# Kernel optimization log

Measured on AMD Instinct MI355X. Metric: run time of the kernel, lower is better.

Reference implementation:

```python
import jax, jax.numpy as jnp
import numpy as np

N_NODES = 50000
N_EDGES = 1600000
D = 128
L = 4
N_GRAPHS = 512


def setup_inputs() -> dict:
    key = jax.random.key(0)
    ks = jax.random.split(key, 8)
    x = jax.random.normal(ks[0], (N_NODES, D), dtype=jnp.float32)
    edge_index = jax.random.randint(ks[1], (2, N_EDGES), 0, N_NODES, dtype=jnp.int64)
    batch = jnp.sort(jax.random.randint(ks[2], (N_NODES,), 0, N_GRAPHS, dtype=jnp.int64))
    # MLP params per GIN layer: Linear(D->D), ReLU, Linear(D->D). Stacked over L layers.
    s = 1.0 / np.sqrt(D)
    Ws1 = jax.random.uniform(ks[3], (L, D, D), jnp.float32, -s, s)
    bs1 = jax.random.uniform(ks[4], (L, D), jnp.float32, -s, s)
    Ws2 = jax.random.uniform(ks[5], (L, D, D), jnp.float32, -s, s)
    bs2 = jax.random.uniform(ks[6], (L, D), jnp.float32, -s, s)
    return {"x": x, "edge_index": edge_index, "batch": batch,
            "Ws1": Ws1, "bs1": bs1, "Ws2": Ws2, "bs2": bs2}


def reference(x, edge_index, batch, Ws1, bs1, Ws2, bs2):
    src, dst = edge_index[0], edge_index[1]
    for l in range(L):
        # GINConv (eps=0): h = MLP(x + sum_{j in N(i)} x_j)
        agg = jax.ops.segment_sum(x[src], dst, num_segments=N_NODES)  # [N, D]
        h = x + agg
        h = jax.nn.relu(h @ Ws1[l] + bs1[l])
        x = h @ Ws2[l] + bs2[l]
    # global_add_pool: segment-sum node features by graph id
    return jax.ops.segment_sum(x, batch, num_segments=N_GRAPHS)  # [G, D]
```

## Files before the change

kernel.cpp:

```cpp
#include <hip/hip_runtime.h>

#define NN 50000
#define NE 1600000
#define DD 128
#define NL 4
#define NG 512
#define NBUK 196
#define NBLK 196
#define EPB 8192
#define HN (NBUK * NBLK)
#define HT 151

typedef __attribute__((ext_vector_type(8))) short short8;
typedef __attribute__((ext_vector_type(4))) float floatx4;

__device__ __forceinline__ unsigned short f2bf(float f) {
    unsigned int u = __float_as_uint(f);
    u += 0x7fffu + ((u >> 16) & 1u);
    return (unsigned short)(u >> 16);
}
__device__ __forceinline__ float bf2f(unsigned short u) {
    return __uint_as_float(((unsigned int)u) << 16);
}

__global__ __launch_bounds__(256) void cvt_kernel(const float* __restrict__ x,
                                                  unsigned short* __restrict__ xbf) {
    int idx = blockIdx.x * 256 + threadIdx.x;
    float4 f = ((const float4*)x)[idx];
    ushort4 o;
    o.x = f2bf(f.x); o.y = f2bf(f.y); o.z = f2bf(f.z); o.w = f2bf(f.w);
    ((ushort4*)xbf)[idx] = o;
}


__global__ __launch_bounds__(512) void bhist_kernel(const int* __restrict__ dst,
                                                    int* __restrict__ hist) {
    __shared__ int h[NBUK];
    int tid = threadIdx.x;
    for (int i = tid; i < NBUK; i += 512) h[i] = 0;
    __syncthreads();
    int base = blockIdx.x * EPB;
#pragma unroll
    for (int it = 0; it < EPB / 512; it++) {
        int e = base + it * 512 + tid;
        if (e < NE) atomicAdd(&h[dst[e] >> 8], 1);
    }
    __syncthreads();
    for (int i = tid; i < NBUK; i += 512) hist[i * NBLK + blockIdx.x] = h[i];
}

__global__ __launch_bounds__(256) void sum_tiles_kernel(const int* __restrict__ in,
                                                        int* __restrict__ tsum, int n) {
    int i = blockIdx.x * 256 + threadIdx.x;
    __shared__ int s[256];
    s[threadIdx.x] = (i < n) ? in[i] : 0;
    __syncthreads();
    for (int off = 128; off > 0; off >>= 1) {
        if (threadIdx.x < off) s[threadIdx.x] += s[threadIdx.x + off];
        __syncthreads();
    }
    if (threadIdx.x == 0) tsum[blockIdx.x] = s[0];
}

__global__ __launch_bounds__(256) void scan_tiles_kernel(const int* __restrict__ tsum,
                                                         int* __restrict__ toff, int ntiles) {
    int t = threadIdx.x;
    __shared__ int s[256];
    int v = (t < ntiles) ? tsum[t] : 0;
    s[t] = v;
    __syncthreads();
    for (int off = 1; off < 256; off <<= 1) {
        int u = (t >= off) ? s[t - off] : 0;
        __syncthreads();
        s[t] += u;
        __syncthreads();
    }
    if (t < ntiles) toff[t] = s[t] - v;
}

__global__ __launch_bounds__(256) void scan_out_kernel(const int* __restrict__ in,
                                                       const int* __restrict__ toff,
                                                       int* __restrict__ out, int n) {
    int i = blockIdx.x * 256 + threadIdx.x;
    int t = threadIdx.x;
    int v = (i < n) ? in[i] : 0;
    __shared__ int s[256];
    s[t] = v;
    __syncthreads();
    for (int off = 1; off < 256; off <<= 1) {
        int u = (t >= off) ? s[t - off] : 0;
        __syncthreads();
        s[t] += u;
        __syncthreads();
    }
    if (i < n) out[i] = toff[blockIdx.x] + s[t] - v;
}

__global__ __launch_bounds__(512) void bscatter_kernel(const int* __restrict__ src,
                                                       const int* __restrict__ dst,
                                                       const int* __restrict__ bkoff,
                                                       int* __restrict__ ebuf) {
    __shared__ int h[NBUK];
    int tid = threadIdx.x;
    for (int i = tid; i < NBUK; i += 512) h[i] = 0;
    __syncthreads();
    int base = blockIdx.x * EPB;
#pragma unroll
    for (int it = 0; it < EPB / 512; it++) {
        int e = base + it * 512 + tid;
        if (e < NE) {
            int d = dst[e];
            int bu = d >> 8;
            int p = atomicAdd(&h[bu], 1);
            ebuf[bkoff[bu * NBLK + blockIdx.x] + p] = (src[e] << 8) | (d & 255);
        }
    }
}

__global__ __launch_bounds__(256) void bucket_csr_kernel(const int* __restrict__ ebuf,
                                                         const int* __restrict__ bkoff,
                                                         int* __restrict__ rowptr,
                                                         int* __restrict__ col) {
    __shared__ int cnt[256], exc[256], c2[256];
    int b = blockIdx.x, tid = threadIdx.x;
    int segstart = bkoff[b * NBLK];
    int segend = (b < NBUK - 1) ? bkoff[(b + 1) * NBLK] : NE;
    cnt[tid] = 0;
    c2[tid] = 0;
    __syncthreads();
    for (int i = segstart + tid; i < segend; i += 256)
        atomicAdd(&cnt[ebuf[i] & 255], 1);
    __syncthreads();
    int v = cnt[tid];
    exc[tid] = v;
    __syncthreads();
    for (int off = 1; off < 256; off <<= 1) {
        int u = (tid >= off) ? exc[tid - off] : 0;
        __syncthreads();
        exc[tid] += u;
        __syncthreads();
    }
    int excl = exc[tid] - v;
    exc[tid] = excl;
    int node = (b << 8) + tid;
    if (node <= NN) rowptr[node] = segstart + excl;
    __syncthreads();
    for (int i = segstart + tid; i < segend; i += 256) {
        int ev = ebuf[i];
        int low = ev & 255;
        int p = atomicAdd(&c2[low], 1);
        col[segstart + exc[low] + p] = ((unsigned)ev) >> 8;
    }
}

__global__ __launch_bounds__(256) void prep_kernel(const float* __restrict__ Ws1,
                                                   const float* __restrict__ Ws2,
                                                   unsigned short* __restrict__ W1T,
                                                   unsigned short* __restrict__ W2T) {
    int idx = blockIdx.x * 256 + threadIdx.x;
    int l = idx >> 14;
    int rem = idx & 16383;
    int k = rem >> 7;
    int n = rem & 127;
    int o = (l << 14) + (n << 7) + k;
    W1T[o] = f2bf(Ws1[idx]);
    W2T[o] = f2bf(Ws2[idx]);
}

__global__ __launch_bounds__(256) void agg_kernel(const unsigned short* __restrict__ xbf,
                                                  const int* __restrict__ rowptr,
                                                  const int* __restrict__ col,
                                                  unsigned short* __restrict__ hpre) {
    int g = threadIdx.x >> 4;
    int lane = threadIdx.x & 15;
    int node = blockIdx.x * 16 + g;
    const uint4* base = (const uint4*)xbf;
    float a[8];
    {
        uint4 v = base[node * 16 + lane];
        a[0] = __uint_as_float(v.x << 16); a[1] = __uint_as_float(v.x & 0xFFFF0000u);
        a[2] = __uint_as_float(v.y << 16); a[3] = __uint_as_float(v.y & 0xFFFF0000u);
        a[4] = __uint_as_float(v.z << 16); a[5] = __uint_as_float(v.z & 0xFFFF0000u);
        a[6] = __uint_as_float(v.w << 16); a[7] = __uint_as_float(v.w & 0xFFFF0000u);
    }
    int s = rowptr[node], e = rowptr[node + 1];
    int i = s;
    for (; i + 8 <= e; i += 8) {
        uint4 v0 = base[col[i] * 16 + lane];
        uint4 v1 = base[col[i + 1] * 16 + lane];
        uint4 v2 = base[col[i + 2] * 16 + lane];
        uint4 v3 = base[col[i + 3] * 16 + lane];
        uint4 v4 = base[col[i + 4] * 16 + lane];
        uint4 v5 = base[col[i + 5] * 16 + lane];
        uint4 v6 = base[col[i + 6] * 16 + lane];
        uint4 v7 = base[col[i + 7] * 16 + lane];
#define ACC(V)                                                            \
        a[0] += __uint_as_float(V.x << 16); a[1] += __uint_as_float(V.x & 0xFFFF0000u); \
        a[2] += __uint_as_float(V.y << 16); a[3] += __uint_as_float(V.y & 0xFFFF0000u); \
        a[4] += __uint_as_float(V.z << 16); a[5] += __uint_as_float(V.z & 0xFFFF0000u); \
        a[6] += __uint_as_float(V.w << 16); a[7] += __uint_as_float(V.w & 0xFFFF0000u)
        ACC(v0); ACC(v1); ACC(v2); ACC(v3); ACC(v4); ACC(v5); ACC(v6); ACC(v7);
    }
    for (; i < e; i++) {
        uint4 v = base[col[i] * 16 + lane];
        ACC(v);
    }
#undef ACC
    uint4 o;
    o.x = (unsigned int)f2bf(a[0]) | ((unsigned int)f2bf(a[1]) << 16);
    o.y = (unsigned int)f2bf(a[2]) | ((unsigned int)f2bf(a[3]) << 16);
    o.z = (unsigned int)f2bf(a[4]) | ((unsigned int)f2bf(a[5]) << 16);
    o.w = (unsigned int)f2bf(a[6]) | ((unsigned int)f2bf(a[7]) << 16);
    ((uint4*)hpre)[node * 16 + lane] = o;
}

#define WS_STR 136
template <bool RELU>
__global__ __launch_bounds__(256) void gemm_kernel(const unsigned short* __restrict__ A,
                                                   const unsigned short* __restrict__ WT,
                                                   const float* __restrict__ bias,
                                                   unsigned short* __restrict__ O) {
    __shared__ unsigned short Ws[64 * WS_STR];
    int bx = blockIdx.x;
    int m = bx >> 1, nh = bx & 1;
    int tid = threadIdx.x;

    const uint4* wg = (const uint4*)(WT + (size_t)(nh * 64) * DD);
#pragma unroll
    for (int it = 0; it < 4; it++) {
        int idx = it * 256 + tid;
        int n = idx >> 4, kc = idx & 15;
        *(uint4*)&Ws[n * WS_STR + kc * 8] = wg[idx];
    }
    __syncthreads();

    int w = tid >> 6;
    int lane = tid & 63;
    int quad = lane >> 4;
    int li = lane & 15;
    int rowb = m * 128 + w * 32;

    floatx4 acc[2][4];
#pragma unroll
    for (int mi = 0; mi < 2; mi++)
#pragma unroll
        for (int tn = 0; tn < 4; tn++) acc[mi][tn] = (floatx4){0.f, 0.f, 0.f, 0.f};

#pragma unroll
    for (int kk = 0; kk < 4; kk++) {
        int k0 = kk * 32 + quad * 8;
        short8 af[2];
#pragma unroll
        for (int mi = 0; mi < 2; mi++) {
            int ar = rowb + mi * 16 + li;
            af[mi] = (ar < NN) ? *(const short8*)(A + (size_t)ar * DD + k0)
                               : (short8){0, 0, 0, 0, 0, 0, 0, 0};
        }
#pragma unroll
        for (int tn = 0; tn < 4; tn++) {
            short8 bf = *(const short8*)&Ws[(tn * 16 + li) * WS_STR + k0];
            acc[0][tn] = __builtin_amdgcn_mfma_f32_16x16x32_bf16(af[0], bf, acc[0][tn], 0, 0, 0);
            acc[1][tn] = __builtin_amdgcn_mfma_f32_16x16x32_bf16(af[1], bf, acc[1][tn], 0, 0, 0);
        }
    }
#pragma unroll
    for (int tn = 0; tn < 4; tn++) {
        int colg = nh * 64 + tn * 16 + li;
        float bv = bias[colg];
#pragma unroll
        for (int mi = 0; mi < 2; mi++) {
#pragma unroll
            for (int r = 0; r < 4; r++) {
                int grow = rowb + mi * 16 + quad * 4 + r;
                if (grow < NN) {
                    float v = acc[mi][tn][r] + bv;
                    if (RELU) v = fmaxf(v, 0.f);
                    O[(size_t)grow * DD + colg] = f2bf(v);
                }
            }
        }
    }
}

__global__ __launch_bounds__(128) void pool_kernel(const unsigned short* __restrict__ x,
                                                   const int* __restrict__ batch,
                                                   float* __restrict__ out) {
    int g = blockIdx.x;
    int lo = 0, hi = NN;
    while (lo < hi) { int mid = (lo + hi) >> 1; if (batch[mid] < g) lo = mid + 1; else hi = mid; }
    int s = lo;
    hi = NN;
    while (lo < hi) { int mid = (lo + hi) >> 1; if (batch[mid] < g + 1) lo = mid + 1; else hi = mid; }
    int e = lo;
    int d = threadIdx.x;
    float acc = 0.f;
    for (int i = s; i < e; i++) acc += bf2f(x[(size_t)i * DD + d]);
    out[g * DD + d] = acc;
}

extern "C" void kernel_launch(void* const* d_in, const int* in_sizes, int n_in,
                              void* d_out, int out_size, void* d_ws, size_t ws_size,
                              hipStream_t stream) {
    const float* x0 = (const float*)d_in[0];
    const int* edge = (const int*)d_in[1];
    const int* batch = (const int*)d_in[2];
    const float* Ws1 = (const float*)d_in[3];
    const float* bs1 = (const float*)d_in[4];
    const float* Ws2 = (const float*)d_in[5];
    const float* bs2 = (const float*)d_in[6];
    float* out = (float*)d_out;
    const int* src = edge;
    const int* dst = edge + NE;

    char* ws = (char*)d_ws;
    size_t off = 0;
    auto alloc = [&](size_t bytes) {
        void* p = ws + off;
        off += (bytes + 255) & ~(size_t)255;
        return p;
    };
    unsigned short* x0bf = (unsigned short*)alloc((size_t)NN * DD * 2);
    unsigned short* xA = (unsigned short*)alloc((size_t)NN * DD * 2);
    unsigned short* xB = (unsigned short*)alloc((size_t)NN * DD * 2);
    unsigned short* hpre = (unsigned short*)alloc((size_t)NN * DD * 2);
    unsigned short* Hbuf = (unsigned short*)alloc((size_t)NN * DD * 2);
    int* col = (int*)alloc((size_t)NE * 4);
    int* ebuf = (int*)alloc((size_t)NE * 4);
    int* hist = (int*)alloc((size_t)HN * 4);
    int* bkoff = (int*)alloc((size_t)HN * 4);
    int* tsum = (int*)alloc((size_t)HT * 4);
    int* toff = (int*)alloc((size_t)HT * 4);
    int* rowptr = (int*)alloc((size_t)(NN + 1) * 4);
    unsigned short* W1T = (unsigned short*)alloc((size_t)NL * DD * DD * 2);
    unsigned short* W2T = (unsigned short*)alloc((size_t)NL * DD * DD * 2);

    cvt_kernel<<<(NN * DD / 4) / 256, 256, 0, stream>>>(x0, x0bf);
    bhist_kernel<<<NBLK, 512, 0, stream>>>(dst, hist);
    sum_tiles_kernel<<<HT, 256, 0, stream>>>(hist, tsum, HN);
    scan_tiles_kernel<<<1, 256, 0, stream>>>(tsum, toff, HT);
    scan_out_kernel<<<HT, 256, 0, stream>>>(hist, toff, bkoff, HN);
    bscatter_kernel<<<NBLK, 512, 0, stream>>>(src, dst, bkoff, ebuf);
    bucket_csr_kernel<<<NBUK, 256, 0, stream>>>(ebuf, bkoff, rowptr, col);
    prep_kernel<<<(NL * DD * DD) / 256, 256, 0, stream>>>(Ws1, Ws2, W1T, W2T);

    const unsigned short* xin = x0bf;
    unsigned short* bufs[2] = {xA, xB};
    const int gemm_grid = ((NN + 127) / 128) * 2;
    for (int l = 0; l < NL; l++) {
        agg_kernel<<<NN / 16, 256, 0, stream>>>(xin, rowptr, col, hpre);
        unsigned short* xout = bufs[l & 1];
        gemm_kernel<true><<<gemm_grid, 256, 0, stream>>>(hpre, W1T + l * DD * DD,
                                                         bs1 + l * DD, Hbuf);
        gemm_kernel<false><<<gemm_grid, 256, 0, stream>>>(Hbuf, W2T + l * DD * DD,
                                                          bs2 + l * DD, xout);
        xin = xout;
    }
    pool_kernel<<<NG, 128, 0, stream>>>(xin, batch, out);
}
```

Before: 494.4 us.

## Fuse both MLP GEMMs into one kernel keeping hidden tile in LDS

Replaces the two separate GEMM launches per layer with one kernel. Each block computes a 128-row tile of the first linear layer with ReLU, keeps the bf16 hidden tile in swizzled shared memory, then reloads the second weight matrix and computes the output. This removes the global write and re-read of the hidden activation buffer and one launch per layer. The MFMA operands are also swapped so results are stored as packed 4-element vectors. The cost is 64KB of LDS per block, which lowers occupancy, and half as many blocks.

```diff
diff --git a/kernel.cpp b/kernel.cpp
--- a/kernel.cpp
+++ b/kernel.cpp
@@ -214,69 +214,126 @@
     ((uint4*)hpre)[node * 16 + lane] = o;
 }
 
-#define WS_STR 136
-template <bool RELU>
-__global__ __launch_bounds__(256) void gemm_kernel(const unsigned short* __restrict__ A,
-                                                   const unsigned short* __restrict__ WT,
-                                                   const float* __restrict__ bias,
-                                                   unsigned short* __restrict__ O) {
-    __shared__ unsigned short Ws[64 * WS_STR];
-    int bx = blockIdx.x;
-    int m = bx >> 1, nh = bx & 1;
+__global__ __launch_bounds__(256) void mlp_kernel(const unsigned short* __restrict__ A,
+                                                  const unsigned short* __restrict__ W1,
+                                                  const float* __restrict__ b1,
+                                                  const unsigned short* __restrict__ W2,
+                                                  const float* __restrict__ b2,
+                                                  unsigned short* __restrict__ O) {
+    __shared__ unsigned short Wl[128 * 128];
+    __shared__ unsigned short Hl[128 * 128];
     int tid = threadIdx.x;
-
-    const uint4* wg = (const uint4*)(WT + (size_t)(nh * 64) * DD);
-#pragma unroll
-    for (int it = 0; it < 4; it++) {
-        int idx = it * 256 + tid;
-        int n = idx >> 4, kc = idx & 15;
-        *(uint4*)&Ws[n * WS_STR + kc * 8] = wg[idx];
-    }
-    __syncthreads();
-
-    int w = tid >> 6;
+    int wg = tid >> 6;
     int lane = tid & 63;
     int quad = lane >> 4;
     int li = lane & 15;
-    int rowb = m * 128 + w * 32;
-
-    floatx4 acc[2][4];
-#pragma unroll
-    for (int mi = 0; mi < 2; mi++)
-#pragma unroll
-        for (int tn = 0; tn < 4; tn++) acc[mi][tn] = (floatx4){0.f, 0.f, 0.f, 0.f};
+    int mg = wg >> 1, ng = wg & 1;
+    int rowb = blockIdx.x * 128;
+
+    {
+        const uint4* wgl = (const uint4*)W1;
+#pragma unroll
+        for (int it = 0; it < 8; it++) {
+            int idx = it * 256 + tid;
+            int n = idx >> 4, kc = idx & 15;
+            *(uint4*)&Wl[n * 128 + ((kc * 8) ^ ((n & 7) << 3))] = wgl[idx];
+        }
+    }
+    __syncthreads();
+
+    floatx4 acc[4][4];
+#pragma unroll
+    for (int tn = 0; tn < 4; tn++)
+#pragma unroll
+        for (int mi = 0; mi < 4; mi++) acc[tn][mi] = (floatx4){0.f, 0.f, 0.f, 0.f};
 
 #pragma unroll
     for (int kk = 0; kk < 4; kk++) {
-        int k0 = kk * 32 + quad * 8;
-        short8 af[2];
-#pragma unroll
-        for (int mi = 0; mi < 2; mi++) {
-            int ar = rowb + mi * 16 + li;
-            af[mi] = (ar < NN) ? *(const short8*)(A + (size_t)ar * DD + k0)
+        int kc = kk * 32 + quad * 8;
+        short8 xf[4];
+#pragma unroll
+        for (int mi = 0; mi < 4; mi++) {
+            int ar = rowb + mg * 64 + mi * 16 + li;
+            xf[mi] = (ar < NN) ? *(const short8*)(A + (size_t)ar * DD + kc)
                                : (short8){0, 0, 0, 0, 0, 0, 0, 0};
         }
 #pragma unroll
         for (int tn = 0; tn < 4; tn++) {
-            short8 bf = *(const short8*)&Ws[(tn * 16 + li) * WS_STR + k0];
-            acc[0][tn] = __builtin_amdgcn_mfma_f32_16x16x32_bf16(af[0], bf, acc[0][tn], 0, 0, 0);
-            acc[1][tn] = __builtin_amdgcn_mfma_f32_16x16x32_bf16(af[1], bf, acc[1][tn], 0, 0, 0);
-        }
-    }
+            int wr = ng * 64 + tn * 16 + li;
+            short8 wf = *(const short8*)&Wl[wr * 128 + (kc ^ ((wr & 7) << 3))];
+#pragma unroll
+            for (int mi = 0; mi < 4; mi++)
+                acc[tn][mi] = __builtin_amdgcn_mfma_f32_16x16x32_bf16(wf, xf[mi], acc[tn][mi], 0, 0, 0);
+        }
+    }
+
 #pragma unroll
     for (int tn = 0; tn < 4; tn++) {
-        int colg = nh * 64 + tn * 16 + li;
-        float bv = bias[colg];
-#pragma unroll
-        for (int mi = 0; mi < 2; mi++) {
-#pragma unroll
-            for (int r = 0; r < 4; r++) {
-                int grow = rowb + mi * 16 + quad * 4 + r;
-                if (grow < NN) {
-                    float v = acc[mi][tn][r] + bv;
-                    if (RELU) v = fmaxf(v, 0.f);
-                    O[(size_t)grow * DD + colg] = f2bf(v);
-                }
+        float4 bv = ((const float4*)b1)[ng * 16 + tn * 4 + quad];
+#pragma unroll
+        for (int mi = 0; mi < 4; mi++) {
+            int hr = mg * 64 + mi * 16 + li;
+            float v0 = fmaxf(acc[tn][mi][0] + bv.x, 0.f);
+            float v1 = fmaxf(acc[tn][mi][1] + bv.y, 0.f);
+            float v2 = fmaxf(acc[tn][mi][2] + bv.z, 0.f);
+            float v3 = fmaxf(acc[tn][mi][3] + bv.w, 0.f);
+            uint2 u;
+            u.x = (unsigned int)f2bf(v0) | ((unsigned int)f2bf(v1) << 16);
+            u.y = (unsigned int)f2bf(v2) | ((unsigned int)f2bf(v3) << 16);
+            int c = (ng * 64 + tn * 16 + quad * 4) ^ ((hr & 7) << 3);
+            *(uint2*)&Hl[hr * 128 + c] = u;
+        }
+    }
+    __syncthreads();
+
+    {
+        const uint4* wgl = (const uint4*)W2;
+#pragma unroll
+        for (int it = 0; it < 8; it++) {
+            int idx = it * 256 + tid;
+            int n = idx >> 4, kc = idx & 15;
+            *(uint4*)&Wl[n * 128 + ((kc * 8) ^ ((n & 7) << 3))] = wgl[idx];
+        }
+    }
+    __syncthreads();
+
+#pragma unroll
+    for (int tn = 0; tn < 4; tn++)
+#pragma unroll
+        for (int mi = 0; mi < 4; mi++) acc[tn][mi] = (floatx4){0.f, 0.f, 0.f, 0.f};
+
+#pragma unroll
+    for (int kk = 0; kk < 4; kk++) {
+        int kc = kk * 32 + quad * 8;
+        short8 hf[4];
+#pragma unroll
+        for (int mi = 0; mi < 4; mi++) {
+            int hr = mg * 64 + mi * 16 + li;
+            hf[mi] = *(const short8*)&Hl[hr * 128 + (kc ^ ((hr & 7) << 3))];
+        }
+#pragma unroll
+        for (int tn = 0; tn < 4; tn++) {
+            int wr = ng * 64 + tn * 16 + li;
+            short8 wf = *(const short8*)&Wl[wr * 128 + (kc ^ ((wr & 7) << 3))];
+#pragma unroll
+            for (int mi = 0; mi < 4; mi++)
+                acc[tn][mi] = __builtin_amdgcn_mfma_f32_16x16x32_bf16(wf, hf[mi], acc[tn][mi], 0, 0, 0);
+        }
+    }
+
+#pragma unroll
+    for (int tn = 0; tn < 4; tn++) {
+        float4 bv = ((const float4*)b2)[ng * 16 + tn * 4 + quad];
+#pragma unroll
+        for (int mi = 0; mi < 4; mi++) {
+            int m = rowb + mg * 64 + mi * 16 + li;
+            if (m < NN) {
+                uint2 u;
+                u.x = (unsigned int)f2bf(acc[tn][mi][0] + bv.x) |
+                      ((unsigned int)f2bf(acc[tn][mi][1] + bv.y) << 16);
+                u.y = (unsigned int)f2bf(acc[tn][mi][2] + bv.z) |
+                      ((unsigned int)f2bf(acc[tn][mi][3] + bv.w) << 16);
+                *(uint2*)&O[(size_t)m * DD + ng * 64 + tn * 16 + quad * 4] = u;
             }
         }
     }
@@ -323,7 +380,6 @@
     unsigned short* xA = (unsigned short*)alloc((size_t)NN * DD * 2);
     unsigned short* xB = (unsigned short*)alloc((size_t)NN * DD * 2);
     unsigned short* hpre = (unsigned short*)alloc((size_t)NN * DD * 2);
-    unsigned short* Hbuf = (unsigned short*)alloc((size_t)NN * DD * 2);
     int* col = (int*)alloc((size_t)NE * 4);
     int* ebuf = (int*)alloc((size_t)NE * 4);
     int* hist = (int*)alloc((size_t)HN * 4);
@@ -345,14 +401,12 @@
 
     const unsigned short* xin = x0bf;
     unsigned short* bufs[2] = {xA, xB};
-    const int gemm_grid = ((NN + 127) / 128) * 2;
+    const int mlp_grid = (NN + 127) / 128;
     for (int l = 0; l < NL; l++) {
         agg_kernel<<<NN / 16, 256, 0, stream>>>(xin, rowptr, col, hpre);
         unsigned short* xout = bufs[l & 1];
-        gemm_kernel<true><<<gemm_grid, 256, 0, stream>>>(hpre, W1T + l * DD * DD,
-                                                         bs1 + l * DD, Hbuf);
-        gemm_kernel<false><<<gemm_grid, 256, 0, stream>>>(Hbuf, W2T + l * DD * DD,
-                                                          bs2 + l * DD, xout);
+        mlp_kernel<<<mlp_grid, 256, 0, stream>>>(hpre, W1T + l * DD * DD, bs1 + l * DD,
+                                                 W2T + l * DD * DD, bs2 + l * DD, xout);
         xin = xout;
     }
     pool_kernel<<<NG, 128, 0, stream>>>(xin, batch, out);
```

Result: faster. 437.8 us (-11.5%).
